# Kernel optimization log

Measured on AMD Instinct MI355X. Metric: run time of the kernel, lower is better.

## Reference

```python
import jax, jax.numpy as jnp
import numpy as np

BETA = 1.0
MIN_FEATURE_SIZE = 1.0
NX_RHO, NY_RHO = 32, 32          # control-point grid
NX_PHI, NY_PHI = 480, 240        # level-set evaluation grid (mirrored to 480x480)


def setup_inputs() -> dict:
    key = jax.random.key(0)
    params = jax.random.normal(key, (NX_RHO * NY_RHO,), dtype=jnp.float32)
    x_rho = jnp.linspace(0.0, 1.0, NX_RHO, dtype=jnp.float32)
    y_rho = jnp.linspace(0.0, 1.0, NY_RHO, dtype=jnp.float32)
    x_phi = jnp.linspace(0.0, 1.0, NY_PHI, dtype=jnp.float32)  # len == ny_phi
    y_phi = jnp.linspace(0.0, 1.0, NX_PHI, dtype=jnp.float32)  # len == nx_phi
    return {
        "params": params,
        "x_rho": x_rho, "y_rho": y_rho,
        "x_phi": x_phi, "y_phi": y_phi,
        "nx_phi": NX_PHI, "ny_phi": NY_PHI,
        "rho_size": 1.0 / NX_RHO,      # RBF sigma
        "grid_size": 1.0 / NX_PHI,     # finite-difference spacing
    }


def _points(xv, yv):
    # torch.meshgrid(yv, xv, indexing='ij'); column_stack((first.flat, second.flat))
    Y, X = jnp.meshgrid(yv, xv, indexing="ij")  # [Ny, Nx]
    return jnp.stack([Y.ravel(), X.ravel()], axis=1)  # [Ny*Nx, 2]


def _gauss(pi, pj, sig):
    # exp(-d^2 / (2 sig^2)); skip the sqrt->square round-trip (same forward math)
    d2 = (pi[:, None, 0] - pj[None, :, 0]) ** 2 + (pi[:, None, 1] - pj[None, :, 1]) ** 2
    return jnp.exp(-d2 / (2.0 * sig ** 2))


def _grad1d(phi, d, axis):
    # central diff interior, one-sided at the two borders (matches the torch loop)
    p = jnp.moveaxis(phi, axis, 0)
    g = jnp.concatenate(
        [(p[1:2] - p[0:1]) / d,
         (p[2:] - p[:-2]) / (2.0 * d),
         (p[-1:] - p[-2:-1]) / d], axis=0)
    return jnp.moveaxis(g, 0, axis)


def reference(params, x_rho, y_rho, x_phi, y_phi, nx_phi, ny_phi, rho_size, grid_size):
    # level-set RBF interpolation
    xy0 = _points(x_rho, y_rho)                    # [Nrho, 2]
    K = _gauss(xy0, xy0, rho_size)                 # [Nrho, Nrho]
    model = jnp.linalg.inv(K) @ params             # [Nrho]
    xy1 = _points(x_phi, y_phi)                    # [Nphi, 2]
    phi = _gauss(xy0, xy1, rho_size).T @ model     # [Nphi]
    phi = phi.reshape(nx_phi, ny_phi)
    phi = jnp.concatenate([phi, phi[:, ::-1]], axis=1)  # mirror along y

    SC = 1e-12
    phi_x = _grad1d(phi, grid_size, 0) + SC
    phi_y = _grad1d(phi, grid_size, 1) + SC
    phi_xx = _grad1d(phi_x, grid_size, 0)
    phi_xy = _grad1d(phi_x, grid_size, 1)
    phi_yy = _grad1d(phi_y, grid_size, 1)

    pi_d = np.pi / (1.3 * MIN_FEATURE_SIZE)
    phi_v = jnp.maximum(jnp.sqrt(phi_x ** 2 + phi_y ** 2), 1e-8)
    phi_vv = (phi_x ** 2 * phi_xx + 2.0 * phi_x * phi_y * phi_xy + phi_y ** 2 * phi_yy) / phi_v ** 2
    pen = jnp.maximum(jnp.abs(phi_vv) / (pi_d * jnp.abs(phi) + BETA * phi_v) - pi_d, 0.0)
    return jnp.nansum(pen * grid_size ** 2)
```

## Files before the change

### kernel.cpp

```cpp
#include <hip/hip_runtime.h>
#include <math.h>

#define NR    32
#define NXPHI 480
#define NYPHI 240
#define NFULL 480
#define TI    32
#define TJ    32

#define WS_MODEL 0

__global__ __launch_bounds__(1024)
void k_solve(const float* __restrict__ params,
             const float* __restrict__ x_rho,
             const float* __restrict__ y_rho,
             const float* __restrict__ rho_size,
             float* __restrict__ ws,
             float* __restrict__ out)
{
    __shared__ double Ay[NR][NR + 1];
    __shared__ double Ax[NR][NR + 1];
    __shared__ double Ry[NR][NR + 1];
    __shared__ double Rx[NR][NR + 1];

    const int t = threadIdx.x;
    const int r = t >> 5;
    const int c = t & 31;

    if (t == 0) out[0] = 0.0f;

    const double sig    = (double)rho_size[0];
    const double inv2s2 = 1.0 / (2.0 * sig * sig);

    {
        double dy = (double)y_rho[r] - (double)y_rho[c];
        double dx = (double)x_rho[r] - (double)x_rho[c];
        Ay[r][c] = exp(-dy * dy * inv2s2);
        Ax[r][c] = exp(-dx * dx * inv2s2);
        double id = (r == c) ? 1.0 : 0.0;
        Ry[r][c] = id;
        Rx[r][c] = id;
    }
    __syncthreads();

    for (int k = 0; k < NR; ++k) {
        double fy = Ay[r][k] / Ay[k][k];
        double fx = Ax[r][k] / Ax[k][k];
        __syncthreads();
        if (r != k) {
            Ay[r][c] -= fy * Ay[k][c];
            Ry[r][c] -= fy * Ry[k][c];
            Ax[r][c] -= fx * Ax[k][c];
            Rx[r][c] -= fx * Rx[k][c];
        }
        __syncthreads();
    }

    const double iay = 1.0 / Ay[r][r];
    const double iax = 1.0 / Ax[r][r];
    Ry[r][c] *= iay;
    Rx[r][c] *= iax;
    __syncthreads();

    double m1 = 0.0;
    #pragma unroll
    for (int b = 0; b < NR; ++b)
        m1 += (double)params[r * NR + b] * Rx[b][c];
    Ay[r][c] = m1;
    __syncthreads();

    double mo = 0.0;
    #pragma unroll
    for (int b = 0; b < NR; ++b)
        mo += Ry[r][b] * Ay[b][c];
    ws[WS_MODEL + r * NR + c] = (float)mo;
}

__global__ __launch_bounds__(256)
void k_fused(const float* __restrict__ x_rho,
             const float* __restrict__ y_rho,
             const float* __restrict__ x_phi,
             const float* __restrict__ y_phi,
             const float* __restrict__ rho_size,
             const float* __restrict__ grid_size,
             const float* __restrict__ model,
             float* __restrict__ out)
{
    __shared__ float sM [NR][NR];
    __shared__ float sGy[TI + 4][NR + 1];
    __shared__ float sGx[TJ + 4][NR + 1];
    __shared__ float sT [TI + 4][NR + 1];
    __shared__ float sP [TI + 4][TJ + 5];

    const int tid = threadIdx.x;
    const int i0  = blockIdx.y * TI;
    const int j0  = blockIdx.x * TJ;

    const float sig    = rho_size[0];
    const float inv2s2 = 1.0f / (2.0f * sig * sig);
    const float d      = grid_size[0];
    const float invd   = 1.0f / d;
    const float inv2d  = 0.5f * invd;

    for (int idx = tid; idx < NR * NR; idx += 256)
        (&sM[0][0])[idx] = model[idx];

    for (int idx = tid; idx < (TI + 4) * NR; idx += 256) {
        const int li = idx >> 5;
        const int a  = idx & 31;
        const int gi = i0 - 2 + li;
        if (gi >= 0 && gi < NFULL) {
            float dy = y_phi[gi] - y_rho[a];
            sGy[li][a] = expf(-dy * dy * inv2s2);
        }
        const int gj = j0 - 2 + li;
        if (gj >= 0) {
            int jm = (gj < NYPHI) ? gj : (NFULL - 1 - gj);
            float dx = x_phi[jm] - x_rho[a];
            sGx[li][a] = expf(-dx * dx * inv2s2);
        }
    }
    __syncthreads();

    for (int idx = tid; idx < (TI + 4) * NR; idx += 256) {
        const int li = idx >> 5;
        const int b  = idx & 31;
        const int gi = i0 - 2 + li;
        if (gi >= 0 && gi < NFULL) {
            float s = 0.0f;
            #pragma unroll
            for (int a = 0; a < NR; ++a) s += sGy[li][a] * sM[a][b];
            sT[li][b] = s;
        }
    }
    __syncthreads();

    for (int idx = tid; idx < (TI + 4) * (TJ + 4); idx += 256) {
        const int li = idx / (TJ + 4);
        const int lj = idx - li * (TJ + 4);
        const int gi = i0 - 2 + li;
        const int gj = j0 - 2 + lj;
        if (gi >= 0 && gi < NFULL && gj >= 0) {
            float s = 0.0f;
            #pragma unroll
            for (int b = 0; b < NR; ++b) s += sT[li][b] * sGx[lj][b];
            sP[li][lj] = s;
        }
    }
    __syncthreads();

    auto PH = [&](int gi, int gj) -> float {
        return sP[gi - i0 + 2][gj - j0 + 2];
    };
    auto GA = [&](int gi, int gj) -> float {
        if (gi == 0)         return (PH(1, gj)         - PH(0, gj))         * invd;
        if (gi == NFULL - 1) return (PH(NFULL-1, gj)   - PH(NFULL-2, gj))   * invd;
        return (PH(gi + 1, gj) - PH(gi - 1, gj)) * inv2d;
    };
    auto GB = [&](int gi, int gj) -> float {
        if (gj == 0)         return (PH(gi, 1)         - PH(gi, 0))         * invd;
        if (gj == NFULL - 1) return (PH(gi, NFULL-1)   - PH(gi, NFULL-2))   * invd;
        return (PH(gi, gj + 1) - PH(gi, gj - 1)) * inv2d;
    };

    const float SC  = 1e-12f;
    const float pid = (float)(3.14159265358979323846 / 1.3);

    float acc = 0.0f;
    for (int p = tid; p < TI * TJ; p += 256) {
        const int li = p >> 5;
        const int lj = p & 31;
        const int gi = i0 + li;
        const int gj = j0 + lj;
        if (gi < NFULL && gj < NYPHI) {
            const float u_c = GA(gi, gj);
            const float v_c = GB(gi, gj);
            const float px = u_c + SC;
            const float py = v_c + SC;

            float pxx, pxy, pyy;
            if (gi == 0)              pxx = (GA(1, gj) - u_c) * invd;
            else if (gi == NFULL - 1) pxx = (u_c - GA(NFULL - 2, gj)) * invd;
            else                      pxx = (GA(gi + 1, gj) - GA(gi - 1, gj)) * inv2d;

            if (gj == 0)              pxy = (GA(gi, 1) - u_c) * invd;
            else if (gj == NFULL - 1) pxy = (u_c - GA(gi, NFULL - 2)) * invd;
            else                      pxy = (GA(gi, gj + 1) - GA(gi, gj - 1)) * inv2d;

            if (gj == 0)              pyy = (GB(gi, 1) - v_c) * invd;
            else if (gj == NFULL - 1) pyy = (v_c - GB(gi, NFULL - 2)) * invd;
            else                      pyy = (GB(gi, gj + 1) - GB(gi, gj - 1)) * inv2d;

            float phiv = fmaxf(sqrtf(px * px + py * py), 1e-8f);
            const float phivv = (px * px * pxx + 2.0f * px * py * pxy + py * py * pyy)
                                / (phiv * phiv);
            float pen = fmaxf(fabsf(phivv) / (pid * fabsf(PH(gi, gj)) + phiv) - pid, 0.0f);
            if (isnan(pen)) pen = 0.0f;
            acc += pen;
        }
    }

    acc *= 2.0f * d * d;

    #pragma unroll
    for (int o = 32; o > 0; o >>= 1) acc += __shfl_down(acc, o, 64);
    __shared__ float wsum[4];
    const int lane = tid & 63;
    const int w    = tid >> 6;
    if (lane == 0) wsum[w] = acc;
    __syncthreads();
    if (tid == 0) atomicAdd(out, wsum[0] + wsum[1] + wsum[2] + wsum[3]);
}

extern "C" void kernel_launch(void* const* d_in, const int* in_sizes, int n_in,
                              void* d_out, int out_size, void* d_ws, size_t ws_size,
                              hipStream_t stream)
{
    const float* params    = (const float*)d_in[0];
    const float* x_rho     = (const float*)d_in[1];
    const float* y_rho     = (const float*)d_in[2];
    const float* x_phi     = (const float*)d_in[3];
    const float* y_phi     = (const float*)d_in[4];
    const float* rho_size  = (const float*)d_in[7];
    const float* grid_size = (const float*)d_in[8];

    float* out = (float*)d_out;
    float* ws  = (float*)d_ws;

    hipLaunchKernelGGL(k_solve, dim3(1), dim3(1024), 0, stream,
                       params, x_rho, y_rho, rho_size, ws, out);
    hipLaunchKernelGGL(k_fused, dim3((NYPHI + TJ - 1) / TJ, NFULL / TI), dim3(256), 0, stream,
                       x_rho, y_rho, x_phi, y_phi, rho_size, grid_size,
                       ws + WS_MODEL, out);
}
```

Measured before the change: 102.9 us.

## Fuse RBF solve into stencil kernel with redundant fp32 per-block inversion

Removes the separate single-block fp64 solve kernel and has every block redundantly invert the separable 32x32 kernel factors in fp32 with fast reciprocals and exp. The output is zeroed via a memset, and the tile width shrinks to 16 so the grid evenly covers the domain without bounds checks. This is meant to eliminate the serialized small solve kernel and its launch dependency, at the cost of duplicated work per block and reduced numerical precision in an unpivoted inversion.

```diff
diff --git a/kernel.cpp b/kernel.cpp
--- a/kernel.cpp
+++ b/kernel.cpp
@@ -2,99 +2,34 @@
 #include <math.h>
 
 #define NR    32
-#define NXPHI 480
 #define NYPHI 240
 #define NFULL 480
 #define TI    32
-#define TJ    32
-
-#define WS_MODEL 0
-
-__global__ __launch_bounds__(1024)
-void k_solve(const float* __restrict__ params,
-             const float* __restrict__ x_rho,
-             const float* __restrict__ y_rho,
-             const float* __restrict__ rho_size,
-             float* __restrict__ ws,
-             float* __restrict__ out)
+#define TJ    16
+#define GRID_I (NFULL / TI)
+#define GRID_J (NYPHI / TJ)
+
+__global__ __launch_bounds__(256)
+void k_all(const float* __restrict__ params,
+           const float* __restrict__ x_rho,
+           const float* __restrict__ y_rho,
+           const float* __restrict__ x_phi,
+           const float* __restrict__ y_phi,
+           const float* __restrict__ rho_size,
+           const float* __restrict__ grid_size,
+           float* __restrict__ out)
 {
-    __shared__ double Ay[NR][NR + 1];
-    __shared__ double Ax[NR][NR + 1];
-    __shared__ double Ry[NR][NR + 1];
-    __shared__ double Rx[NR][NR + 1];
-
-    const int t = threadIdx.x;
-    const int r = t >> 5;
-    const int c = t & 31;
-
-    if (t == 0) out[0] = 0.0f;
-
-    const double sig    = (double)rho_size[0];
-    const double inv2s2 = 1.0 / (2.0 * sig * sig);
-
-    {
-        double dy = (double)y_rho[r] - (double)y_rho[c];
-        double dx = (double)x_rho[r] - (double)x_rho[c];
-        Ay[r][c] = exp(-dy * dy * inv2s2);
-        Ax[r][c] = exp(-dx * dx * inv2s2);
-        double id = (r == c) ? 1.0 : 0.0;
-        Ry[r][c] = id;
-        Rx[r][c] = id;
-    }
-    __syncthreads();
-
-    for (int k = 0; k < NR; ++k) {
-        double fy = Ay[r][k] / Ay[k][k];
-        double fx = Ax[r][k] / Ax[k][k];
-        __syncthreads();
-        if (r != k) {
-            Ay[r][c] -= fy * Ay[k][c];
-            Ry[r][c] -= fy * Ry[k][c];
-            Ax[r][c] -= fx * Ax[k][c];
-            Rx[r][c] -= fx * Rx[k][c];
-        }
-        __syncthreads();
-    }
-
-    const double iay = 1.0 / Ay[r][r];
-    const double iax = 1.0 / Ax[r][r];
-    Ry[r][c] *= iay;
-    Rx[r][c] *= iax;
-    __syncthreads();
-
-    double m1 = 0.0;
-    #pragma unroll
-    for (int b = 0; b < NR; ++b)
-        m1 += (double)params[r * NR + b] * Rx[b][c];
-    Ay[r][c] = m1;
-    __syncthreads();
-
-    double mo = 0.0;
-    #pragma unroll
-    for (int b = 0; b < NR; ++b)
-        mo += Ry[r][b] * Ay[b][c];
-    ws[WS_MODEL + r * NR + c] = (float)mo;
-}
-
-__global__ __launch_bounds__(256)
-void k_fused(const float* __restrict__ x_rho,
-             const float* __restrict__ y_rho,
-             const float* __restrict__ x_phi,
-             const float* __restrict__ y_phi,
-             const float* __restrict__ rho_size,
-             const float* __restrict__ grid_size,
-             const float* __restrict__ model,
-             float* __restrict__ out)
-{
-    __shared__ float sM [NR][NR];
+    __shared__ float Ay[NR][NR + 1], Ax[NR][NR + 1];
+    __shared__ float Ry[NR][NR + 1], Rx[NR][NR + 1];
+    __shared__ float sM [NR][NR + 1];
     __shared__ float sGy[TI + 4][NR + 1];
     __shared__ float sGx[TJ + 4][NR + 1];
     __shared__ float sT [TI + 4][NR + 1];
     __shared__ float sP [TI + 4][TJ + 5];
 
     const int tid = threadIdx.x;
-    const int i0  = blockIdx.y * TI;
-    const int j0  = blockIdx.x * TJ;
+    const int c   = tid & 31;
+    const int w   = tid >> 5;
 
     const float sig    = rho_size[0];
     const float inv2s2 = 1.0f / (2.0f * sig * sig);
@@ -102,22 +37,88 @@
     const float invd   = 1.0f / d;
     const float inv2d  = 0.5f * invd;
 
-    for (int idx = tid; idx < NR * NR; idx += 256)
-        (&sM[0][0])[idx] = model[idx];
+    #pragma unroll
+    for (int q = 0; q < 4; ++q) {
+        const int r = w + 8 * q;
+        const float dy = y_rho[r] - y_rho[c];
+        const float dx = x_rho[r] - x_rho[c];
+        Ay[r][c] = __expf(-dy * dy * inv2s2);
+        Ax[r][c] = __expf(-dx * dx * inv2s2);
+        const float id = (r == c) ? 1.0f : 0.0f;
+        Ry[r][c] = id;
+        Rx[r][c] = id;
+    }
+    __syncthreads();
+
+    for (int k = 0; k < NR; ++k) {
+        const float iay = __builtin_amdgcn_rcpf(Ay[k][k]);
+        const float iax = __builtin_amdgcn_rcpf(Ax[k][k]);
+        float fy[4], fx[4];
+        #pragma unroll
+        for (int q = 0; q < 4; ++q) {
+            const int r = w + 8 * q;
+            fy[q] = Ay[r][k] * iay;
+            fx[q] = Ax[r][k] * iax;
+        }
+        __syncthreads();
+        #pragma unroll
+        for (int q = 0; q < 4; ++q) {
+            const int r = w + 8 * q;
+            if (r != k) {
+                Ay[r][c] -= fy[q] * Ay[k][c];
+                Ry[r][c] -= fy[q] * Ry[k][c];
+                Ax[r][c] -= fx[q] * Ax[k][c];
+                Rx[r][c] -= fx[q] * Rx[k][c];
+            }
+        }
+        __syncthreads();
+    }
+
+    #pragma unroll
+    for (int q = 0; q < 4; ++q) {
+        const int r = w + 8 * q;
+        Ry[r][c] *= __builtin_amdgcn_rcpf(Ay[r][r]);
+        Rx[r][c] *= __builtin_amdgcn_rcpf(Ax[r][r]);
+    }
+    __syncthreads();
+
+    #pragma unroll
+    for (int q = 0; q < 4; ++q) {
+        const int r = w + 8 * q;
+        float s = 0.0f;
+        #pragma unroll
+        for (int b = 0; b < NR; ++b) s += params[r * NR + b] * Rx[b][c];
+        Ay[r][c] = s;
+    }
+    __syncthreads();
+
+    #pragma unroll
+    for (int q = 0; q < 4; ++q) {
+        const int r = w + 8 * q;
+        float s = 0.0f;
+        #pragma unroll
+        for (int b = 0; b < NR; ++b) s += Ry[r][b] * Ay[b][c];
+        sM[r][c] = s;
+    }
+
+    const int i0 = blockIdx.y * TI;
+    const int j0 = blockIdx.x * TJ;
 
     for (int idx = tid; idx < (TI + 4) * NR; idx += 256) {
         const int li = idx >> 5;
         const int a  = idx & 31;
         const int gi = i0 - 2 + li;
         if (gi >= 0 && gi < NFULL) {
-            float dy = y_phi[gi] - y_rho[a];
-            sGy[li][a] = expf(-dy * dy * inv2s2);
-        }
-        const int gj = j0 - 2 + li;
-        if (gj >= 0) {
-            int jm = (gj < NYPHI) ? gj : (NFULL - 1 - gj);
-            float dx = x_phi[jm] - x_rho[a];
-            sGx[li][a] = expf(-dx * dx * inv2s2);
+            const float dy = y_phi[gi] - y_rho[a];
+            sGy[li][a] = __expf(-dy * dy * inv2s2);
+        }
+        if (li < TJ + 4) {
+            const int gj = j0 - 2 + li;
+            if (gj >= 0) {
+                const int jm = (gj < NYPHI) ? gj : (NFULL - 1 - gj);
+                const float dx = x_phi[jm] - x_rho[a];
+                sGx[li][a] = __expf(-dx * dx * inv2s2);
+            }
         }
     }
     __syncthreads();
@@ -153,13 +154,13 @@
         return sP[gi - i0 + 2][gj - j0 + 2];
     };
     auto GA = [&](int gi, int gj) -> float {
-        if (gi == 0)         return (PH(1, gj)         - PH(0, gj))         * invd;
-        if (gi == NFULL - 1) return (PH(NFULL-1, gj)   - PH(NFULL-2, gj))   * invd;
+        if (gi == 0)         return (PH(1, gj)       - PH(0, gj))       * invd;
+        if (gi == NFULL - 1) return (PH(NFULL-1, gj) - PH(NFULL-2, gj)) * invd;
         return (PH(gi + 1, gj) - PH(gi - 1, gj)) * inv2d;
     };
     auto GB = [&](int gi, int gj) -> float {
-        if (gj == 0)         return (PH(gi, 1)         - PH(gi, 0))         * invd;
-        if (gj == NFULL - 1) return (PH(gi, NFULL-1)   - PH(gi, NFULL-2))   * invd;
+        if (gj == 0)         return (PH(gi, 1)       - PH(gi, 0))       * invd;
+        if (gj == NFULL - 1) return (PH(gi, NFULL-1) - PH(gi, NFULL-2)) * invd;
         return (PH(gi, gj + 1) - PH(gi, gj - 1)) * inv2d;
     };
 
@@ -167,37 +168,36 @@
     const float pid = (float)(3.14159265358979323846 / 1.3);
 
     float acc = 0.0f;
-    for (int p = tid; p < TI * TJ; p += 256) {
-        const int li = p >> 5;
-        const int lj = p & 31;
+    #pragma unroll
+    for (int p = 0; p < 2; ++p) {
+        const int px_idx = tid + p * 256;
+        const int li = px_idx >> 4;
+        const int lj = px_idx & 15;
         const int gi = i0 + li;
         const int gj = j0 + lj;
-        if (gi < NFULL && gj < NYPHI) {
-            const float u_c = GA(gi, gj);
-            const float v_c = GB(gi, gj);
-            const float px = u_c + SC;
-            const float py = v_c + SC;
-
-            float pxx, pxy, pyy;
-            if (gi == 0)              pxx = (GA(1, gj) - u_c) * invd;
-            else if (gi == NFULL - 1) pxx = (u_c - GA(NFULL - 2, gj)) * invd;
-            else                      pxx = (GA(gi + 1, gj) - GA(gi - 1, gj)) * inv2d;
-
-            if (gj == 0)              pxy = (GA(gi, 1) - u_c) * invd;
-            else if (gj == NFULL - 1) pxy = (u_c - GA(gi, NFULL - 2)) * invd;
-            else                      pxy = (GA(gi, gj + 1) - GA(gi, gj - 1)) * inv2d;
-
-            if (gj == 0)              pyy = (GB(gi, 1) - v_c) * invd;
-            else if (gj == NFULL - 1) pyy = (v_c - GB(gi, NFULL - 2)) * invd;
-            else                      pyy = (GB(gi, gj + 1) - GB(gi, gj - 1)) * inv2d;
-
-            float phiv = fmaxf(sqrtf(px * px + py * py), 1e-8f);
-            const float phivv = (px * px * pxx + 2.0f * px * py * pxy + py * py * pyy)
-                                / (phiv * phiv);
-            float pen = fmaxf(fabsf(phivv) / (pid * fabsf(PH(gi, gj)) + phiv) - pid, 0.0f);
-            if (isnan(pen)) pen = 0.0f;
-            acc += pen;
-        }
+
+        const float u_c = GA(gi, gj);
+        const float v_c = GB(gi, gj);
+        const float pxv = u_c + SC;
+        const float pyv = v_c + SC;
+
+        float pxx, pxy, pyy;
+        if (gi == 0)              pxx = (GA(1, gj) - u_c) * invd;
+        else if (gi == NFULL - 1) pxx = (u_c - GA(NFULL - 2, gj)) * invd;
+        else                      pxx = (GA(gi + 1, gj) - GA(gi - 1, gj)) * inv2d;
+
+        if (gj == 0)              pxy = (GA(gi, 1) - u_c) * invd;
+        else                      pxy = (GA(gi, gj + 1) - GA(gi, gj - 1)) * inv2d;
+
+        if (gj == 0)              pyy = (GB(gi, 1) - v_c) * invd;
+        else                      pyy = (GB(gi, gj + 1) - GB(gi, gj - 1)) * inv2d;
+
+        const float phiv  = fmaxf(sqrtf(pxv * pxv + pyv * pyv), 1e-8f);
+        const float phivv = (pxv * pxv * pxx + 2.0f * pxv * pyv * pxy + pyv * pyv * pyy)
+                            / (phiv * phiv);
+        float pen = fmaxf(fabsf(phivv) / (pid * fabsf(PH(gi, gj)) + phiv) - pid, 0.0f);
+        if (isnan(pen)) pen = 0.0f;
+        acc += pen;
     }
 
     acc *= 2.0f * d * d;
@@ -206,8 +206,8 @@
     for (int o = 32; o > 0; o >>= 1) acc += __shfl_down(acc, o, 64);
     __shared__ float wsum[4];
     const int lane = tid & 63;
-    const int w    = tid >> 6;
-    if (lane == 0) wsum[w] = acc;
+    const int wv   = tid >> 6;
+    if (lane == 0) wsum[wv] = acc;
     __syncthreads();
     if (tid == 0) atomicAdd(out, wsum[0] + wsum[1] + wsum[2] + wsum[3]);
 }
@@ -225,11 +225,9 @@
     const float* grid_size = (const float*)d_in[8];
 
     float* out = (float*)d_out;
-    float* ws  = (float*)d_ws;
-
-    hipLaunchKernelGGL(k_solve, dim3(1), dim3(1024), 0, stream,
-                       params, x_rho, y_rho, rho_size, ws, out);
-    hipLaunchKernelGGL(k_fused, dim3((NYPHI + TJ - 1) / TJ, NFULL / TI), dim3(256), 0, stream,
-                       x_rho, y_rho, x_phi, y_phi, rho_size, grid_size,
-                       ws + WS_MODEL, out);
+
+    hipMemsetAsync(out, 0, sizeof(float), stream);
+    hipLaunchKernelGGL(k_all, dim3(GRID_J, GRID_I), dim3(256), 0, stream,
+                       params, x_rho, y_rho, x_phi, y_phi,
+                       rho_size, grid_size, out);
 }
```

Result: faster. 99.62 us (-3.2%).
